# Optimization experiments

Measured on AMD Instinct MI355X. Metric: run time of the kernel, lower is better.

The kernel has to match this reference:

```python
import jax, jax.numpy as jnp
import numpy as np

NU = 160000   # users
NM = 60000    # movies
D = 64        # embedding dim
E = 5000000   # rating edges
L = 200000    # label edges to score
NUM_LAYERS = 3


def setup_inputs() -> dict:
    key = jax.random.key(0)
    k1, k2, k3, k4, k5, k6 = jax.random.split(key, 6)
    return {
        "emb_user": jax.random.normal(k1, (NU, D), jnp.float32),
        "emb_movie": jax.random.normal(k2, (NM, D), jnp.float32),
        "node_id_user": jnp.arange(NU),
        "node_id_movie": jnp.arange(NM),
        "edge_from": jax.random.randint(k3, (E,), 0, NM),   # movie side of each edge
        "edge_to": jax.random.randint(k4, (E,), 0, NU),     # user side of each edge
        "label_movie": jax.random.randint(k5, (L,), 0, NM),
        "label_user": jax.random.randint(k6, (L,), 0, NU),
    }


def reference(emb_user, emb_movie, node_id_user, node_id_movie,
              edge_from, edge_to, label_movie, label_user):
    # Embedding lookup (node_id is an arange over all nodes in the batch)
    x_u = emb_user[node_id_user]    # [NU, D]
    x_m = emb_movie[node_id_movie]  # [NM, D]

    # Symmetric degree normalization: deg(from)^-1/2 * deg(to)^-1/2 per edge
    ones = jnp.ones(edge_from.shape[0], dtype=x_m.dtype)
    deg_m = jax.ops.segment_sum(ones, edge_from, num_segments=NM)
    deg_u = jax.ops.segment_sum(ones, edge_to, num_segments=NU)
    inv_m = jnp.where(deg_m > 0, deg_m ** -0.5, 0.0)
    inv_u = jnp.where(deg_u > 0, deg_u ** -0.5, 0.0)
    norm = inv_m[edge_from] * inv_u[edge_to]  # [E]

    # NOTE: the original torch code never writes the propagated embeddings back
    # into x_dict, so every layer propagates the layer-0 embeddings. Replicated
    # faithfully here.
    embs_u = [x_u]
    embs_m = [x_m]
    for _ in range(NUM_LAYERS):
        # movie -> user aggregation (x2y): gather movie feats, scale, scatter-add to users
        u_agg = jax.ops.segment_sum(norm[:, None] * x_m[edge_from], edge_to, num_segments=NU)
        m_agg = jax.ops.segment_sum(norm[:, None] * x_u[edge_to], edge_from, num_segments=NM)
        embs_u.append(u_agg)
        embs_m.append(m_agg)

    # Layer combination with weights 1/(l+1)
    w = 1.0 / (jnp.arange(NUM_LAYERS + 1, dtype=x_u.dtype) + 1.0)
    res_u = jnp.einsum('l,lnd->nd', w, jnp.stack(embs_u))  # [NU, D]
    res_m = jnp.einsum('l,lnd->nd', w, jnp.stack(embs_m))  # [NM, D]

    # Classifier: dot product over label edges
    scores = jnp.sum(res_u[label_user] * res_m[label_movie], axis=-1)  # [L]
    return (scores, res_u, res_m)
```

## Files before the change

### kernel.cpp

```cpp
#include <hip/hip_runtime.h>
#include <hip/hip_bf16.h>

#define NU 160000
#define NM 60000
#define DD 64
#define NE 5000000
#define NL 200000

#define COEF (13.0f / 12.0f)

#define SHIFT_U 9
#define SHIFT_M 7
#define NBU ((NU + (1 << SHIFT_U) - 1) >> SHIFT_U)
#define NBM ((NM + (1 << SHIFT_M) - 1) >> SHIFT_M)
#define VB_U 16
#define VB_M 18

#define UDIV 30000
#define LG_U 1
#define MDIV 27000
#define LG_M 3
#define NPASS_U 2
#define NPASS_M 6
#define NVU (NU << LG_U)
#define NVM (NM << LG_M)
#define BS 1024


#define CEC 16

__global__ void bucket_count_kernel(const int* __restrict__ ef, const int* __restrict__ et,
                                    int* __restrict__ gbh_u, int* __restrict__ gbh_m) {
    __shared__ int bhu[NBU], bhm[NBM];
    int tid = threadIdx.x;
    for (int i = tid; i < NBU; i += 256) bhu[i] = 0;
    for (int i = tid; i < NBM; i += 256) bhm[i] = 0;
    __syncthreads();
    int base = (blockIdx.x * 256 + tid) * CEC;
    if (base < NE) {
        const int4* f4 = (const int4*)(ef + base);
        const int4* t4 = (const int4*)(et + base);
        #pragma unroll
        for (int q = 0; q < CEC / 4; q++) {
            int4 ff = f4[q]; int4 tt = t4[q];
            atomicAdd(&bhm[ff.x >> SHIFT_M], 1); atomicAdd(&bhu[tt.x >> SHIFT_U], 1);
            atomicAdd(&bhm[ff.y >> SHIFT_M], 1); atomicAdd(&bhu[tt.y >> SHIFT_U], 1);
            atomicAdd(&bhm[ff.z >> SHIFT_M], 1); atomicAdd(&bhu[tt.z >> SHIFT_U], 1);
            atomicAdd(&bhm[ff.w >> SHIFT_M], 1); atomicAdd(&bhu[tt.w >> SHIFT_U], 1);
        }
    }
    __syncthreads();
    for (int i = tid; i < NBU; i += 256) if (bhu[i]) atomicAdd(&gbh_u[i], bhu[i]);
    for (int i = tid; i < NBM; i += 256) if (bhm[i]) atomicAdd(&gbh_m[i], bhm[i]);
}


__global__ void scan_small_kernel(const int* __restrict__ in, int* __restrict__ out,
                                  int* __restrict__ cur, int n) {
    __shared__ int buf[256];
    int tid = threadIdx.x;
    int idx = tid * 4;
    int v0 = (idx + 0 < n) ? in[idx + 0] : 0;
    int v1 = (idx + 1 < n) ? in[idx + 1] : 0;
    int v2 = (idx + 2 < n) ? in[idx + 2] : 0;
    int v3 = (idx + 3 < n) ? in[idx + 3] : 0;
    int s = v0 + v1 + v2 + v3;
    buf[tid] = s;
    __syncthreads();
    for (int off = 1; off < 256; off <<= 1) {
        int t = (tid >= off) ? buf[tid - off] : 0;
        __syncthreads();
        buf[tid] += t;
        __syncthreads();
    }
    int p = buf[tid] - s;
    if (idx + 0 < n) { out[idx + 0] = p; if (cur) cur[idx + 0] = p; p += v0; }
    if (idx + 1 < n) { out[idx + 1] = p; if (cur) cur[idx + 1] = p; p += v1; }
    if (idx + 2 < n) { out[idx + 2] = p; if (cur) cur[idx + 2] = p; p += v2; }
    if (idx + 3 < n) { out[idx + 3] = p; if (cur) cur[idx + 3] = p; p += v3; }
    if (tid == 255) out[n] = buf[255];
}


#define PEC 16

__global__ void partition_kernel(const int* __restrict__ key, const int* __restrict__ val,
                                 int* __restrict__ bcur, int* __restrict__ stage,
                                 int nb, int valbits, int mode) {
    __shared__ int lh[512];
    __shared__ int lbase[512];
    int tid = threadIdx.x;
    for (int i = tid; i < nb; i += 256) lh[i] = 0;
    __syncthreads();
    int base = (blockIdx.x * 256 + tid) * PEC;
    int kv_[PEC], v_[PEC], br_[PEC];
    bool act = base < NE;
    if (act) {
        int k_[PEC];
        const int4* k4 = (const int4*)(key + base);
        const int4* v4 = (const int4*)(val + base);
        #pragma unroll
        for (int q = 0; q < PEC / 4; q++) {
            int4 kk = k4[q]; int4 vv = v4[q];
            k_[q * 4 + 0] = kk.x; k_[q * 4 + 1] = kk.y; k_[q * 4 + 2] = kk.z; k_[q * 4 + 3] = kk.w;
            v_[q * 4 + 0] = vv.x; v_[q * 4 + 1] = vv.y; v_[q * 4 + 2] = vv.z; v_[q * 4 + 3] = vv.w;
        }
        #pragma unroll
        for (int q = 0; q < PEC; q++) {
            int kv;
            if (mode == 0) kv = (k_[q] << LG_U) | (v_[q] >= UDIV ? 1 : 0);
            else           kv = (k_[q] << LG_M) | (int)((unsigned)v_[q] / MDIV);
            kv_[q] = kv;
            int b = kv >> 10;
            int r = atomicAdd(&lh[b], 1);
            br_[q] = (b << 13) | r;
        }
    }
    __syncthreads();
    for (int i = tid; i < nb; i += 256) lbase[i] = lh[i] ? atomicAdd(&bcur[i], lh[i]) : 0;
    __syncthreads();
    if (act) {
        #pragma unroll
        for (int q = 0; q < PEC; q++) {
            int b = br_[q] >> 13;
            int r = br_[q] & 8191;
            stage[lbase[b] + r] = ((kv_[q] & (BS - 1)) << valbits) | v_[q];
        }
    }
}


__global__ void build_kernel(const int* __restrict__ stage, const int* __restrict__ bo,
                             int* __restrict__ rp, int* __restrict__ pay,
                             int n, int valbits) {
    __shared__ int cnt[BS];
    __shared__ int tmp[BS];
    int b = blockIdx.x;
    int tid = threadIdx.x;
    int base = b << 10;
    int nn = min(BS, n - base);
    int vmask = (1 << valbits) - 1;
    int s0 = bo[b];
    int s1 = bo[b + 1];

    for (int i = tid; i < BS; i += 256) cnt[i] = 0;
    __syncthreads();
    for (int e = s0 + tid; e < s1; e += 256)
        atomicAdd(&cnt[stage[e] >> valbits], 1);
    __syncthreads();
    int ov[4];
    #pragma unroll
    for (int q = 0; q < 4; q++) ov[q] = cnt[tid + q * 256];
    for (int off = 1; off < BS; off <<= 1) {
        int t[4];
        #pragma unroll
        for (int q = 0; q < 4; q++) {
            int i = tid + q * 256;
            t[q] = (i >= off) ? cnt[i - off] : 0;
        }
        __syncthreads();
        #pragma unroll
        for (int q = 0; q < 4; q++) cnt[tid + q * 256] += t[q];
        __syncthreads();
    }
    #pragma unroll
    for (int q = 0; q < 4; q++) {
        int i = tid + q * 256;
        int excl = cnt[i] - ov[q];
        tmp[i] = s0 + excl;
        if (i < nn) rp[base + i] = s0 + excl;
    }
    if (b == 0 && tid == 0) rp[n] = NE;
    __syncthreads();
    for (int e = s0 + tid; e < s1; e += 256) {
        int p = stage[e];
        int pos = atomicAdd(&tmp[p >> valbits], 1);
        pay[pos] = p & vmask;
    }
}


__global__ void inv_from_rp_kernel(const int* __restrict__ rp, float* __restrict__ inv,
                                   int n, int lg) {
    int i = blockIdx.x * blockDim.x + threadIdx.x;
    if (i < n) {
        int d = rp[(i + 1) << lg] - rp[i << lg];
        inv[i] = (d > 0) ? rsqrtf((float)d) : 0.0f;
    }
}


__global__ void prescale_kernel(const float* __restrict__ x, const float* __restrict__ inv,
                                __hip_bfloat16* __restrict__ y, int total) {
    int i = blockIdx.x * blockDim.x + threadIdx.x;
    if (i < total) {
        int node = i >> 6;
        y[i] = __float2bfloat16(inv[node] * x[i]);
    }
}


__global__ void gather_kernel(const int* __restrict__ rp, const int* __restrict__ pay,
                              const float* __restrict__ inv_dst,
                              const __hip_bfloat16* __restrict__ y_src,
                              const float* __restrict__ x_dst,
                              float* __restrict__ res, int n, int lg, int h, int first) {
    int tid = blockIdx.x * blockDim.x + threadIdx.x;
    int node = tid >> 6;
    int lane = threadIdx.x & 63;
    if (node >= n) return;
    int vk = (node << lg) | h;
    int start = rp[vk];
    int end   = rp[vk + 1];
    if (!first && start == end) return;
    float acc = 0.0f;
    for (int i = start; i < end; i += 64) {
        int cnt = min(end - i, 64);
        int nid = (lane < cnt) ? pay[i + lane] : 0;
        int j = 0;
        for (; j + 4 <= cnt; j += 4) {
            int f0 = __shfl(nid, j + 0, 64);
            int f1 = __shfl(nid, j + 1, 64);
            int f2 = __shfl(nid, j + 2, 64);
            int f3 = __shfl(nid, j + 3, 64);
            float a0 = __bfloat162float(y_src[f0 * DD + lane]);
            float a1 = __bfloat162float(y_src[f1 * DD + lane]);
            float a2 = __bfloat162float(y_src[f2 * DD + lane]);
            float a3 = __bfloat162float(y_src[f3 * DD + lane]);
            acc += a0 + a1 + a2 + a3;
        }
        for (; j < cnt; j++) {
            int f0 = __shfl(nid, j, 64);
            acc += __bfloat162float(y_src[f0 * DD + lane]);
        }
    }
    int o = node * DD + lane;
    float basev = first ? x_dst[o] : res[o];
    res[o] = basev + COEF * inv_dst[node] * acc;
}


__global__ void score_kernel(const int* __restrict__ lm, const int* __restrict__ lu,
                             const float* __restrict__ ru, const float* __restrict__ rm,
                             float* __restrict__ scores) {
    int tid = blockIdx.x * blockDim.x + threadIdx.x;
    int l = tid >> 6;
    int d = threadIdx.x & 63;
    if (l < NL) {
        int u = lu[l];
        int m = lm[l];
        float v = ru[u * DD + d] * rm[m * DD + d];
        #pragma unroll
        for (int off = 32; off >= 1; off >>= 1)
            v += __shfl_down(v, off, 64);
        if (d == 0) scores[l] = v;
    }
}


__global__ void degree_kernel_f(const int* __restrict__ ef, const int* __restrict__ et,
                                float* __restrict__ deg_m, float* __restrict__ deg_u) {
    int i = blockIdx.x * blockDim.x + threadIdx.x;
    if (i < NE) {
        atomicAdd(&deg_m[ef[i]], 1.0f);
        atomicAdd(&deg_u[et[i]], 1.0f);
    }
}

__global__ void inv_kernel_f(float* __restrict__ deg, int n) {
    int i = blockIdx.x * blockDim.x + threadIdx.x;
    if (i < n) {
        float d = deg[i];
        deg[i] = (d > 0.0f) ? (1.0f / sqrtf(d)) : 0.0f;
    }
}

__global__ void agg_kernel_f(const int* __restrict__ ef, const int* __restrict__ et,
                             const float* __restrict__ inv_m, const float* __restrict__ inv_u,
                             const float* __restrict__ x_u, const float* __restrict__ x_m,
                             float* __restrict__ res_u, float* __restrict__ res_m) {
    int tid = blockIdx.x * blockDim.x + threadIdx.x;
    int e = tid >> 6;
    int d = tid & 63;
    if (e < NE) {
        int f = ef[e];
        int t = et[e];
        float norm = inv_m[f] * inv_u[t] * COEF;
        atomicAdd(&res_u[t * DD + d], norm * x_m[f * DD + d]);
        atomicAdd(&res_m[f * DD + d], norm * x_u[t * DD + d]);
    }
}

__global__ void add_base_kernel_f(const float* __restrict__ xu, const float* __restrict__ xm,
                                  float* __restrict__ ru, float* __restrict__ rm) {
    int i = blockIdx.x * blockDim.x + threadIdx.x;
    const int nu = NU * DD;
    const int nm = NM * DD;
    if (i < nu) {
        ru[i] += xu[i];
    } else if (i < nu + nm) {
        int j = i - nu;
        rm[j] += xm[j];
    }
}


extern "C" void kernel_launch(void* const* d_in, const int* in_sizes, int n_in,
                              void* d_out, int out_size, void* d_ws, size_t ws_size,
                              hipStream_t stream) {
    const float* emb_user  = (const float*)d_in[0];
    const float* emb_movie = (const float*)d_in[1];
    const int* edge_from   = (const int*)d_in[4];
    const int* edge_to     = (const int*)d_in[5];
    const int* label_movie = (const int*)d_in[6];
    const int* label_user  = (const int*)d_in[7];

    float* out    = (float*)d_out;
    float* scores = out;
    float* res_u  = out + NL;
    float* res_m  = out + NL + (size_t)NU * DD;

    int*   gbh_u  = (int*)d_ws;
    int*   gbh_m  = gbh_u + NBU;
    int*   bo_u   = gbh_m + NBM;
    int*   bcur_u = bo_u + NBU + 1;
    int*   bo_m   = bcur_u + NBU;
    int*   bcur_m = bo_m + NBM + 1;
    float* inv_u  = (float*)(bcur_m + NBM);
    float* inv_m  = inv_u + NU;
    int*   rp_u   = (int*)(inv_m + NM);
    int*   rp_m   = rp_u + NVU + 1;
    int*   pay_u  = rp_m + NVM + 1;
    int*   pay_m  = pay_u + NE;
    int*   ureg   = pay_m + NE;
    int*   stage  = ureg;
    __hip_bfloat16* y_u = (__hip_bfloat16*)ureg;
    __hip_bfloat16* y_m = (__hip_bfloat16*)(ureg + (size_t)NU * DD / 2);

    size_t ysz    = (size_t)(NU + NM) * DD / 2;
    size_t uni    = (size_t)NE > ysz ? (size_t)NE : ysz;
    size_t needed = ((size_t)(ureg - (int*)d_ws) + uni) * sizeof(int);

    if (ws_size >= needed) {
        hipMemsetAsync(gbh_u, 0, (size_t)(NBU + NBM) * sizeof(int), stream);

        bucket_count_kernel<<<(NE / CEC + 255) / 256, 256, 0, stream>>>(
            edge_from, edge_to, gbh_u, gbh_m);
        scan_small_kernel<<<1, 256, 0, stream>>>(gbh_u, bo_u, bcur_u, NBU);
        scan_small_kernel<<<1, 256, 0, stream>>>(gbh_m, bo_m, bcur_m, NBM);

        partition_kernel<<<(NE / PEC + 255) / 256, 256, 0, stream>>>(
            edge_to, edge_from, bcur_u, stage, NBU, VB_U, 0);
        build_kernel<<<NBU, 256, 0, stream>>>(stage, bo_u, rp_u, pay_u, NVU, VB_U);

        partition_kernel<<<(NE / PEC + 255) / 256, 256, 0, stream>>>(
            edge_from, edge_to, bcur_m, stage, NBM, VB_M, 1);
        build_kernel<<<NBM, 256, 0, stream>>>(stage, bo_m, rp_m, pay_m, NVM, VB_M);

        inv_from_rp_kernel<<<(NU + 255) / 256, 256, 0, stream>>>(rp_u, inv_u, NU, LG_U);
        inv_from_rp_kernel<<<(NM + 255) / 256, 256, 0, stream>>>(rp_m, inv_m, NM, LG_M);

        prescale_kernel<<<((size_t)NU * DD + 255) / 256, 256, 0, stream>>>(
            emb_user, inv_u, y_u, NU * DD);
        prescale_kernel<<<((size_t)NM * DD + 255) / 256, 256, 0, stream>>>(
            emb_movie, inv_m, y_m, NM * DD);

        for (int h = 0; h < NPASS_U; h++)
            gather_kernel<<<((size_t)NU * 64 + 255) / 256, 256, 0, stream>>>(
                rp_u, pay_u, inv_u, y_m, emb_user, res_u, NU, LG_U, h, h == 0);
        for (int h = 0; h < NPASS_M; h++)
            gather_kernel<<<((size_t)NM * 64 + 255) / 256, 256, 0, stream>>>(
                rp_m, pay_m, inv_m, y_u, emb_movie, res_m, NM, LG_M, h, h == 0);
    } else {
        float* fdeg_u = (float*)d_ws;
        float* fdeg_m = fdeg_u + NU;
        hipMemsetAsync(res_u, 0, (size_t)(NU + NM) * DD * sizeof(float), stream);
        hipMemsetAsync(fdeg_u, 0, (size_t)(NU + NM) * sizeof(float), stream);
        degree_kernel_f<<<(NE + 255) / 256, 256, 0, stream>>>(edge_from, edge_to, fdeg_m, fdeg_u);
        inv_kernel_f<<<(NU + NM + 255) / 256, 256, 0, stream>>>(fdeg_u, NU + NM);
        agg_kernel_f<<<((size_t)NE * 64 + 255) / 256, 256, 0, stream>>>(
            edge_from, edge_to, fdeg_m, fdeg_u, emb_user, emb_movie, res_u, res_m);
        add_base_kernel_f<<<((NU + NM) * DD + 255) / 256, 256, 0, stream>>>(
            emb_user, emb_movie, res_u, res_m);
    }

    score_kernel<<<((size_t)NL * 64 + 255) / 256, 256, 0, stream>>>(
        label_movie, label_user, res_u, res_m, scores);
}
```

Baseline: 798.5 us.

## Replace multi-pass movie gather with block-local LDS accumulation over 128-movie buckets

The movie-side CSR is reorganized so each 128-movie bucket holds its edges grouped by user-range slice, with the local movie id packed into the payload. A new 1024-thread gather kernel per bucket walks all eight slices, giving waves even shares of edges, and accumulates run-length partial sums into shared memory with LDS atomics. This replaces six separate gather passes with read-modify-write of the result array, and the user side becomes a single pass. The aim is to drop repeated result traffic and load imbalance, at the cost of shared-memory atomics and 32KB LDS per block, which limits occupancy.

```diff
diff --git a/kernel.cpp b/kernel.cpp
--- a/kernel.cpp
+++ b/kernel.cpp
@@ -18,13 +18,10 @@
 
 #define UDIV 30000
 #define LG_U 1
-#define MDIV 27000
-#define LG_M 3
-#define NPASS_U 2
-#define NPASS_M 6
-#define NVU (NU << LG_U)
-#define NVM (NM << LG_M)
+#define MDIV 20000
 #define BS 1024
+#define NVU2 (NBU << 10)
+#define NVM2 (NBM << 10)
 
 
 #define CEC 16
@@ -86,14 +83,14 @@
 
 __global__ void partition_kernel(const int* __restrict__ key, const int* __restrict__ val,
                                  int* __restrict__ bcur, int* __restrict__ stage,
-                                 int nb, int valbits, int mode) {
+                                 int nb, int shift, int valbits, int mode) {
     __shared__ int lh[512];
     __shared__ int lbase[512];
     int tid = threadIdx.x;
     for (int i = tid; i < nb; i += 256) lh[i] = 0;
     __syncthreads();
     int base = (blockIdx.x * 256 + tid) * PEC;
-    int kv_[PEC], v_[PEC], br_[PEC];
+    int lk_[PEC], v_[PEC], br_[PEC];
     bool act = base < NE;
     if (act) {
         int k_[PEC];
@@ -107,11 +104,12 @@
         }
         #pragma unroll
         for (int q = 0; q < PEC; q++) {
-            int kv;
-            if (mode == 0) kv = (k_[q] << LG_U) | (v_[q] >= UDIV ? 1 : 0);
-            else           kv = (k_[q] << LG_M) | (int)((unsigned)v_[q] / MDIV);
-            kv_[q] = kv;
-            int b = kv >> 10;
+            int k = k_[q];
+            int lk;
+            if (mode == 0) lk = ((k & 511) << 1) | (v_[q] >= UDIV ? 1 : 0);
+            else           lk = ((int)((unsigned)v_[q] / MDIV) << 7) | (k & 127);
+            lk_[q] = lk;
+            int b = k >> shift;
             int r = atomicAdd(&lh[b], 1);
             br_[q] = (b << 13) | r;
         }
@@ -124,7 +122,7 @@
         for (int q = 0; q < PEC; q++) {
             int b = br_[q] >> 13;
             int r = br_[q] & 8191;
-            stage[lbase[b] + r] = ((kv_[q] & (BS - 1)) << valbits) | v_[q];
+            stage[lbase[b] + r] = (lk_[q] << valbits) | v_[q];
         }
     }
 }
@@ -132,7 +130,7 @@
 
 __global__ void build_kernel(const int* __restrict__ stage, const int* __restrict__ bo,
                              int* __restrict__ rp, int* __restrict__ pay,
-                             int n, int valbits) {
+                             int n, int valbits, int pmask) {
     __shared__ int cnt[BS];
     __shared__ int tmp[BS];
     int b = blockIdx.x;
@@ -174,8 +172,9 @@
     __syncthreads();
     for (int e = s0 + tid; e < s1; e += 256) {
         int p = stage[e];
-        int pos = atomicAdd(&tmp[p >> valbits], 1);
-        pay[pos] = p & vmask;
+        int k = p >> valbits;
+        int pos = atomicAdd(&tmp[k], 1);
+        pay[pos] = (p & vmask) | ((k & pmask) << valbits);
     }
 }
 
@@ -189,6 +188,20 @@
     }
 }
 
+__global__ void inv_m_from_rp_kernel(const int* __restrict__ rp, float* __restrict__ inv) {
+    int f = blockIdx.x * blockDim.x + threadIdx.x;
+    if (f < NM) {
+        int base = ((f >> 7) << 10) | (f & 127);
+        int d = 0;
+        #pragma unroll
+        for (int h = 0; h < 8; h++) {
+            int idx = base + (h << 7);
+            d += rp[idx + 1] - rp[idx];
+        }
+        inv[f] = (d > 0) ? rsqrtf((float)d) : 0.0f;
+    }
+}
+
 
 __global__ void prescale_kernel(const float* __restrict__ x, const float* __restrict__ inv,
                                 __hip_bfloat16* __restrict__ y, int total) {
@@ -200,19 +213,17 @@
 }
 
 
-__global__ void gather_kernel(const int* __restrict__ rp, const int* __restrict__ pay,
-                              const float* __restrict__ inv_dst,
-                              const __hip_bfloat16* __restrict__ y_src,
-                              const float* __restrict__ x_dst,
-                              float* __restrict__ res, int n, int lg, int h, int first) {
+__global__ void gather_u_kernel(const int* __restrict__ rp, const int* __restrict__ pay,
+                                const float* __restrict__ inv_dst,
+                                const __hip_bfloat16* __restrict__ y_src,
+                                const float* __restrict__ x_dst,
+                                float* __restrict__ res, int n) {
     int tid = blockIdx.x * blockDim.x + threadIdx.x;
     int node = tid >> 6;
     int lane = threadIdx.x & 63;
     if (node >= n) return;
-    int vk = (node << lg) | h;
-    int start = rp[vk];
-    int end   = rp[vk + 1];
-    if (!first && start == end) return;
+    int start = rp[node << LG_U];
+    int end   = rp[(node + 1) << LG_U];
     float acc = 0.0f;
     for (int i = start; i < end; i += 64) {
         int cnt = min(end - i, 64);
@@ -235,8 +246,81 @@
         }
     }
     int o = node * DD + lane;
-    float basev = first ? x_dst[o] : res[o];
-    res[o] = basev + COEF * inv_dst[node] * acc;
+    res[o] = x_dst[o] + COEF * inv_dst[node] * acc;
+}
+
+
+__global__ __launch_bounds__(1024) void gather_m_kernel(
+        const int* __restrict__ rp, const int* __restrict__ pay,
+        const float* __restrict__ inv_dst,
+        const __hip_bfloat16* __restrict__ y_src,
+        const float* __restrict__ x_dst,
+        float* __restrict__ res) {
+    __shared__ float acc[128 * DD];
+    int b = blockIdx.x;
+    int tid = threadIdx.x;
+    int wave = tid >> 6;
+    int lane = tid & 63;
+    for (int i = tid; i < 128 * DD; i += 1024) acc[i] = 0.0f;
+    __syncthreads();
+
+    int vbase = b << 10;
+    const int umask = (1 << VB_M) - 1;
+    float racc = 0.0f;
+    int rm = -1;
+    for (int h = 0; h < 8; h++) {
+        int s0 = rp[vbase + (h << 7)];
+        int s1 = rp[vbase + (h << 7) + 128];
+        int total = s1 - s0;
+        if (total <= 0) continue;
+        int per = (total + 15) >> 4;
+        int e0 = s0 + wave * per;
+        int e1 = min(e0 + per, s1);
+        for (int i = e0; i < e1; i += 64) {
+            int cnt = min(e1 - i, 64);
+            int pv = (lane < cnt) ? pay[i + lane] : 0;
+            int j = 0;
+            for (; j + 4 <= cnt; j += 4) {
+                int p0 = __shfl(pv, j + 0, 64);
+                int p1 = __shfl(pv, j + 1, 64);
+                int p2 = __shfl(pv, j + 2, 64);
+                int p3 = __shfl(pv, j + 3, 64);
+                float a0 = __bfloat162float(y_src[(p0 & umask) * DD + lane]);
+                float a1 = __bfloat162float(y_src[(p1 & umask) * DD + lane]);
+                float a2 = __bfloat162float(y_src[(p2 & umask) * DD + lane]);
+                float a3 = __bfloat162float(y_src[(p3 & umask) * DD + lane]);
+                int m0 = p0 >> VB_M;
+                if (m0 != rm) { if (rm >= 0) atomicAdd(&acc[rm * DD + lane], racc); rm = m0; racc = a0; }
+                else racc += a0;
+                int m1 = p1 >> VB_M;
+                if (m1 != rm) { if (rm >= 0) atomicAdd(&acc[rm * DD + lane], racc); rm = m1; racc = a1; }
+                else racc += a1;
+                int m2 = p2 >> VB_M;
+                if (m2 != rm) { if (rm >= 0) atomicAdd(&acc[rm * DD + lane], racc); rm = m2; racc = a2; }
+                else racc += a2;
+                int m3 = p3 >> VB_M;
+                if (m3 != rm) { if (rm >= 0) atomicAdd(&acc[rm * DD + lane], racc); rm = m3; racc = a3; }
+                else racc += a3;
+            }
+            for (; j < cnt; j++) {
+                int p0 = __shfl(pv, j, 64);
+                float a0 = __bfloat162float(y_src[(p0 & umask) * DD + lane]);
+                int m0 = p0 >> VB_M;
+                if (m0 != rm) { if (rm >= 0) atomicAdd(&acc[rm * DD + lane], racc); rm = m0; racc = a0; }
+                else racc += a0;
+            }
+        }
+    }
+    if (rm >= 0) atomicAdd(&acc[rm * DD + lane], racc);
+    __syncthreads();
+
+    int nn = min(128, NM - (b << 7));
+    int lim = nn * DD;
+    int gbase = (b << 7) * DD;
+    for (int i = tid; i < lim; i += 1024) {
+        int f = (b << 7) + (i >> 6);
+        res[gbase + i] = x_dst[gbase + i] + COEF * inv_dst[f] * acc[i];
+    }
 }
 
 
@@ -329,8 +413,8 @@
     float* inv_u  = (float*)(bcur_m + NBM);
     float* inv_m  = inv_u + NU;
     int*   rp_u   = (int*)(inv_m + NM);
-    int*   rp_m   = rp_u + NVU + 1;
-    int*   pay_u  = rp_m + NVM + 1;
+    int*   rp_m   = rp_u + NVU2 + 1;
+    int*   pay_u  = rp_m + NVM2 + 1;
     int*   pay_m  = pay_u + NE;
     int*   ureg   = pay_m + NE;
     int*   stage  = ureg;
@@ -350,27 +434,25 @@
         scan_small_kernel<<<1, 256, 0, stream>>>(gbh_m, bo_m, bcur_m, NBM);
 
         partition_kernel<<<(NE / PEC + 255) / 256, 256, 0, stream>>>(
-            edge_to, edge_from, bcur_u, stage, NBU, VB_U, 0);
-        build_kernel<<<NBU, 256, 0, stream>>>(stage, bo_u, rp_u, pay_u, NVU, VB_U);
+            edge_to, edge_from, bcur_u, stage, NBU, SHIFT_U, VB_U, 0);
+        build_kernel<<<NBU, 256, 0, stream>>>(stage, bo_u, rp_u, pay_u, NVU2, VB_U, 0);
 
         partition_kernel<<<(NE / PEC + 255) / 256, 256, 0, stream>>>(
-            edge_from, edge_to, bcur_m, stage, NBM, VB_M, 1);
-        build_kernel<<<NBM, 256, 0, stream>>>(stage, bo_m, rp_m, pay_m, NVM, VB_M);
+            edge_from, edge_to, bcur_m, stage, NBM, SHIFT_M, VB_M, 1);
+        build_kernel<<<NBM, 256, 0, stream>>>(stage, bo_m, rp_m, pay_m, NVM2, VB_M, 127);
 
         inv_from_rp_kernel<<<(NU + 255) / 256, 256, 0, stream>>>(rp_u, inv_u, NU, LG_U);
-        inv_from_rp_kernel<<<(NM + 255) / 256, 256, 0, stream>>>(rp_m, inv_m, NM, LG_M);
+        inv_m_from_rp_kernel<<<(NM + 255) / 256, 256, 0, stream>>>(rp_m, inv_m);
 
         prescale_kernel<<<((size_t)NU * DD + 255) / 256, 256, 0, stream>>>(
             emb_user, inv_u, y_u, NU * DD);
         prescale_kernel<<<((size_t)NM * DD + 255) / 256, 256, 0, stream>>>(
             emb_movie, inv_m, y_m, NM * DD);
 
-        for (int h = 0; h < NPASS_U; h++)
-            gather_kernel<<<((size_t)NU * 64 + 255) / 256, 256, 0, stream>>>(
-                rp_u, pay_u, inv_u, y_m, emb_user, res_u, NU, LG_U, h, h == 0);
-        for (int h = 0; h < NPASS_M; h++)
-            gather_kernel<<<((size_t)NM * 64 + 255) / 256, 256, 0, stream>>>(
-                rp_m, pay_m, inv_m, y_u, emb_movie, res_m, NM, LG_M, h, h == 0);
+        gather_u_kernel<<<((size_t)NU * 64 + 255) / 256, 256, 0, stream>>>(
+            rp_u, pay_u, inv_u, y_m, emb_user, res_u, NU);
+        gather_m_kernel<<<NBM, 1024, 0, stream>>>(
+            rp_m, pay_m, inv_m, y_u, emb_movie, res_m);
     } else {
         float* fdeg_u = (float*)d_ws;
         float* fdeg_m = fdeg_u + NU;
```

Result: slower. 867.4 us (+8.6%).
